# Optimization experiments

Hardware: AMD Instinct MI355X
Metric: run time of the kernel (lower is better)

The kernel has to match this reference:

```python
import jax, jax.numpy as jnp
import numpy as np
from jax import lax

# Fixed high-pass biquad coefficients from SpecTransform.__init__ (a0=b0=1)
A_HP = (-1.99599, 0.996)
B_HP = (-2.0, 1.0)


def _biquad(x, b0, b1, b2, a1, a2):
    """Direct-form-I second-order IIR along last axis of x: (B, T).
    y[t] = b0*x[t] + b1*x[t-1] + b2*x[t-2] - a1*y[t-1] - a2*y[t-2]
    Matches torchaudio.functional.biquad (which calls lfilter with
    default clamp=True, clipping the final output to [-1, 1]).
    """
    z = jnp.zeros((x.shape[0],), x.dtype)

    def step(carry, xt):
        x1, x2, y1, y2 = carry
        y = b0 * xt + b1 * x1 + b2 * x2 - a1 * y1 - a2 * y2
        return (xt, x1, y, y1), y

    _, y = lax.scan(step, (z, z, z, z), x.T)  # scan over time, carry over batch
    return jnp.clip(y.T, -1.0, 1.0)


def _chain(sig, coefs):
    # coefs = [a1, a2, b1, b2] from _rand_resp (hoisted out for determinism)
    a1, a2, b1, b2 = coefs[0], coefs[1], coefs[2], coefs[3]
    sig = _biquad(sig, 1.0, B_HP[0], B_HP[1], A_HP[0], A_HP[1])
    sig = _biquad(sig, 1.0, b1, b2, a1, a2)
    return sig


def setup_inputs() -> dict:
    key = jax.random.key(0)
    k1, k2, k3, k4 = jax.random.split(key, 4)
    B, T = 64, 160000  # 64 clips of 10 s @ 16 kHz
    x = jax.random.normal(k1, (B, T), jnp.float32) * 0.1
    n = jax.random.normal(k2, (B, T), jnp.float32) * 0.1
    # 0.75 * (U[0,1) - 0.5), same distribution as _rand_resp
    coef_x = (jax.random.uniform(k3, (4,), jnp.float32) - 0.5) * 0.75
    coef_n = (jax.random.uniform(k4, (4,), jnp.float32) - 0.5) * 0.75
    return {"x": x, "n": n, "coef_x": coef_x, "coef_n": coef_n}


def reference(x, n, coef_x, coef_n):
    return (_chain(x, coef_x), _chain(n, coef_n))
```

## Files before the change

### kernel.cpp

```cpp
#include <hip/hip_runtime.h>
#include <math.h>

#define T_LEN   160000
#define NROW    128
#define CH      32
#define NCH     5000
#define OWNT    20
#define NCH16   10000
#define OWN16   60
#define B16     240
#define TILES16 42
#define NBLK16  (NROW * TILES16)
#define ROW4    40000

#define C1_HP ( 1.99599)
#define C2_HP (-0.996)
#define C1F   ( 1.99599f)
#define C2F   (-0.996f)

#define S1_FLOAT2S (NROW * NCH)
#define M2_BYTE_OFF (S1_FLOAT2S * 8)

#define GLOBAL_AS __attribute__((address_space(1)))
#define SHARED_AS __attribute__((address_space(3)))

__device__ __forceinline__ int sz16(int F) { return F ^ ((F >> 3) & 7); }
__device__ __forceinline__ float clip1f(float v) { return fminf(fmaxf(v, -1.0f), 1.0f); }

__global__ __launch_bounds__(256) void pass_a1(const float* __restrict__ x,
                                               const float* __restrict__ nn,
                                               float2* __restrict__ e1,
                                               const float* __restrict__ cx,
                                               const float* __restrict__ cn,
                                               float4* __restrict__ m2) {
  int g = blockIdx.x * blockDim.x + threadIdx.x;
  if (g < 2) {
    const float* c = g ? cn : cx;
    const float A1c = c[0], A2c = c[1];
    float pm2 = 0.f, pm1 = 0.f, p0 = 1.f;
#pragma unroll
    for (int k = 0; k < 16; ++k) {
      float pn = -A1c * p0 - A2c * pm1;
      pm2 = pm1; pm1 = p0; p0 = pn;
    }
    float m00 = p0, m01 = -A2c * pm1, m10 = pm1, m11 = -A2c * pm2;
    float q00 = m00*m00 + m01*m10, q01 = m00*m01 + m01*m11;
    float q10 = m10*m00 + m11*m10, q11 = m10*m01 + m11*m11;
    float r00 = q00*m00 + q01*m10, r01 = q00*m01 + q01*m11;
    float r10 = q10*m00 + q11*m10, r11 = q10*m01 + q11*m11;
    m2[g*3 + 0] = make_float4(m00, m01, m10, m11);
    m2[g*3 + 1] = make_float4(q00, q01, q10, q11);
    m2[g*3 + 2] = make_float4(r00, r01, r10, r11);
  }
  if (g >= NROW * NCH) return;
  int row = g / NCH, c = g % NCH;
  const float* src = (row < 64) ? (x + (size_t)row * T_LEN)
                                : (nn + (size_t)(row - 64) * T_LEN);
  const float* xp = src + c * CH;
  float x1 = 0.f, x2 = 0.f;
  if (c) { x1 = xp[-1]; x2 = xp[-2]; }
  double y1 = 0.0, y2 = 0.0;
#pragma unroll
  for (int j = 0; j < CH; j += 4) {
    float4 xv = *reinterpret_cast<const float4*>(xp + j);
#define A1STEP(XF) { float xt = (XF); \
    float fir = (xt - 2.f * x1 + x2); \
    double y = fma(C1_HP, y1, fma(C2_HP, y2, (double)fir)); \
    x2 = x1; x1 = xt; y2 = y1; y1 = y; }
    A1STEP(xv.x) A1STEP(xv.y) A1STEP(xv.z) A1STEP(xv.w)
#undef A1STEP
  }
  e1[g] = make_float2((float)y1, (float)y2);
}

__global__ __launch_bounds__(256) void scan_row(const float2* __restrict__ e,
                                                float2* __restrict__ s) {
  __shared__ double wm[4][6];
  const int t = threadIdx.x, row = blockIdx.x;
  const int lane = t & 63, wv = t >> 6;
  double pm2 = 0.0, pm1 = 0.0, p0 = 1.0;
#pragma unroll
  for (int k = 1; k <= CH; ++k) {
    double pn = C1_HP * p0 + C2_HP * pm1;
    pm2 = pm1; pm1 = p0; p0 = pn;
  }
  const double m00 = p0,  m01 = C2_HP * pm1;
  const double m10 = pm1, m11 = C2_HP * pm2;
  const float2* ep = e + (size_t)row * NCH;
  const int base = t * OWNT;
  double f1 = 0.0, f2 = 0.0;
  for (int j = 0; j < OWNT; ++j) {
    int c = base + j;
    float2 ev = (c < NCH) ? ep[c] : make_float2(0.f, 0.f);
    double n1 = m00 * f1 + m01 * f2 + (double)ev.x;
    double n2 = m10 * f1 + m11 * f2 + (double)ev.y;
    f1 = n1; f2 = n2;
  }
  double b00 = m00, b01 = m01, b10 = m10, b11 = m11;
  double r00 = 1.0, r01 = 0.0, r10 = 0.0, r11 = 1.0;
  int ee = OWNT;
  while (ee) {
    if (ee & 1) {
      double t00 = b00 * r00 + b01 * r10, t01 = b00 * r01 + b01 * r11;
      double t10 = b10 * r00 + b11 * r10, t11 = b10 * r01 + b11 * r11;
      r00 = t00; r01 = t01; r10 = t10; r11 = t11;
    }
    double q00 = b00 * b00 + b01 * b10, q01 = b00 * b01 + b01 * b11;
    double q10 = b10 * b00 + b11 * b10, q11 = b10 * b01 + b11 * b11;
    b00 = q00; b01 = q01; b10 = q10; b11 = q11;
    ee >>= 1;
  }
  double P00 = r00, P01 = r01, P10 = r10, P11 = r11, V1 = f1, V2 = f2;
#pragma unroll
  for (int off = 1; off < 64; off <<= 1) {
    double u00 = __shfl_up(P00, off), u01 = __shfl_up(P01, off);
    double u10 = __shfl_up(P10, off), u11 = __shfl_up(P11, off);
    double uv1 = __shfl_up(V1, off),  uv2 = __shfl_up(V2, off);
    if (lane >= off) {
      double nv1 = P00 * uv1 + P01 * uv2 + V1;
      double nv2 = P10 * uv1 + P11 * uv2 + V2;
      double n00 = P00 * u00 + P01 * u10, n01 = P00 * u01 + P01 * u11;
      double n10 = P10 * u00 + P11 * u10, n11 = P10 * u01 + P11 * u11;
      P00 = n00; P01 = n01; P10 = n10; P11 = n11; V1 = nv1; V2 = nv2;
    }
  }
  if (lane == 63) {
    wm[wv][0] = P00; wm[wv][1] = P01; wm[wv][2] = P10; wm[wv][3] = P11;
    wm[wv][4] = V1;  wm[wv][5] = V2;
  }
  __syncthreads();
  double S1 = 0.0, S2 = 0.0;
  for (int w = 0; w < wv; ++w) {
    double n1 = wm[w][0] * S1 + wm[w][1] * S2 + wm[w][4];
    double n2 = wm[w][2] * S1 + wm[w][3] * S2 + wm[w][5];
    S1 = n1; S2 = n2;
  }
  double q00 = __shfl_up(P00, 1), q01 = __shfl_up(P01, 1);
  double q10 = __shfl_up(P10, 1), q11 = __shfl_up(P11, 1);
  double qv1 = __shfl_up(V1, 1),  qv2 = __shfl_up(V2, 1);
  double st1, st2;
  if (lane == 0) { st1 = S1; st2 = S2; }
  else { st1 = q00 * S1 + q01 * S2 + qv1; st2 = q10 * S1 + q11 * S2 + qv2; }
  float2* sp = s + (size_t)row * NCH;
  double s1v = st1, s2v = st2;
  for (int j = 0; j < OWNT; ++j) {
    int c = base + j;
    if (c < NCH) {
      sp[c] = make_float2((float)s1v, (float)s2v);
      float2 ev = ep[c];
      double n1 = m00 * s1v + m01 * s2v + (double)ev.x;
      double n2 = m10 * s1v + m11 * s2v + (double)ev.y;
      s1v = n1; s2v = n2;
    }
  }
}

__global__ __launch_bounds__(256, 8) void emit_kernel(const float* __restrict__ x,
                                                      const float* __restrict__ nn,
                                                      const float2* __restrict__ s1,
                                                      const float* __restrict__ cx,
                                                      const float* __restrict__ cn,
                                                      const float4* __restrict__ m2,
                                                      float* __restrict__ out) {
  __shared__ float4 ws4[1024];
  const int tid = threadIdx.x, lane = tid & 63, wv = tid >> 6;
  const int b = blockIdx.x;
  const int row = b / TILES16, tile = b % TILES16;
  const int W0 = tile * B16 + wv * OWN16;
  const int c = W0 - 4 + lane;
  const float* src = (row < 64) ? x + (size_t)row * T_LEN
                                : nn + (size_t)(row - 64) * T_LEN;
  const float4* src4 = reinterpret_cast<const float4*>(src);
  const float2* srow = s1 + (size_t)row * NCH;
  const float* cf = (row < 64) ? cx : cn;
  const float A1c = cf[0], A2c = cf[1], B1c = cf[2], B2c = cf[3];
  const int fi = (row < 64) ? 0 : 1;
  const float4 M1q = m2[fi*3], M2q = m2[fi*3+1], M3q = m2[fi*3+2];
  const bool cOK = (c >= 0) && (c < NCH16);

  const int WOFF = wv * 256;
  const long base4 = (long)(W0 - 4) * 4;
  const bool interior = (base4 >= 0) && (base4 + 256 <= ROW4);

  if (interior) {
    const int lane_sz = lane ^ ((lane >> 3) & 7);
#pragma unroll
    for (int q = 0; q < 4; ++q) {
      const float4* gp = src4 + base4 + q * 64 + lane_sz;
      __builtin_amdgcn_global_load_lds(
          (const GLOBAL_AS void*)gp,
          (SHARED_AS void*)(ws4 + WOFF + q * 64),
          16, 0, 0);
    }
    asm volatile("s_waitcnt vmcnt(0)" ::: "memory");
  } else {
#pragma unroll
    for (int q = 0; q < 4; ++q) {
      int f = q * 64 + lane;
      long g4 = base4 + f;
      float4 v = make_float4(0.f, 0.f, 0.f, 0.f);
      if (g4 >= 0 && g4 < ROW4) v = src4[g4];
      ws4[WOFF + sz16(f)] = v;
    }
  }

  float4 a[4];
#pragma unroll
  for (int q = 0; q < 4; ++q) a[q] = ws4[WOFF + sz16(lane * 4 + q)];

  float tx  = __shfl_up(a[3].w, 1), ty  = __shfl_up(a[3].z, 1);
  float t2x = __shfl_up(a[3].w, 2), t2y = __shfl_up(a[3].z, 2);

  float x1 = 0.f, x2 = 0.f, y1 = 0.f, y2 = 0.f, v1 = 0.f, v2 = 0.f;
  if (cOK && c > 0) {
    float2 sv = srow[c >> 1];
    y1 = sv.x; y2 = sv.y;
    if ((lane & 1) == 0) {
      if (lane == 0) {
        float2 tp = *reinterpret_cast<const float2*>(src + (long)c * 16 - 2);
        x2 = tp.x; x1 = tp.y;
      } else { x1 = tx; x2 = ty; }
    } else {
      float ax1 = 0.f, ax2 = 0.f;
      if (lane == 1) {
        if (c >= 2) {
          float2 tp = *reinterpret_cast<const float2*>(src + (long)(c - 1) * 16 - 2);
          ax2 = tp.x; ax1 = tp.y;
        }
      } else { ax1 = t2x; ax2 = t2y; }
      float4 p0 = ws4[WOFF + sz16((lane - 1) * 4 + 0)];
      float4 p1 = ws4[WOFF + sz16((lane - 1) * 4 + 1)];
      float4 p2 = ws4[WOFF + sz16((lane - 1) * 4 + 2)];
      float4 p3 = ws4[WOFF + sz16((lane - 1) * 4 + 3)];
#define ADV(XT) { float xt_ = (XT); \
      float fir = (xt_ - 2.f * ax1 + ax2); \
      float yy = fmaf(C1F, y1, fmaf(C2F, y2, fir)); \
      ax2 = ax1; ax1 = xt_; y2 = y1; y1 = yy; }
      ADV(p0.x) ADV(p0.y) ADV(p0.z) ADV(p0.w)
      ADV(p1.x) ADV(p1.y) ADV(p1.z) ADV(p1.w)
      ADV(p2.x) ADV(p2.y) ADV(p2.z) ADV(p2.w)
      ADV(p3.x) ADV(p3.y) ADV(p3.z) ADV(p3.w)
#undef ADV
      x1 = ax1; x2 = ax2;
    }
    v1 = clip1f(y1); v2 = clip1f(y2);
  }

  {
    float xp1 = x1, xp2 = x2;
#pragma unroll
    for (int q = 0; q < 4; ++q) {
      float4 t = a[q];
      float4 f;
      f.x = t.x - 2.f * xp1 + xp2;
      f.y = t.y - 2.f * t.x + xp1;
      f.z = t.z - 2.f * t.y + t.x;
      f.w = t.w - 2.f * t.z + t.y;
      xp2 = t.z; xp1 = t.w;
      a[q] = f;
    }
  }

  float z1 = 0.f, z2 = 0.f;
  if (cOK) {
#define AB(REF) { \
    float yy = fmaf(C1F, y1, fmaf(C2F, y2, (REF))); \
    float vv = clip1f(yy); \
    float zz = fmaf(-A1c, z1, fmaf(-A2c, z2, fmaf(B2c, v2, fmaf(B1c, v1, vv)))); \
    y2 = y1; y1 = yy; v2 = v1; v1 = vv; z2 = z1; z1 = zz; REF = zz; }
#pragma unroll
    for (int q = 0; q < 4; ++q) { AB(a[q].x) AB(a[q].y) AB(a[q].z) AB(a[q].w) }
#undef AB
  }

  float u1x = __shfl_up(z1, 1), u1y = __shfl_up(z2, 1);
  float u2x = __shfl_up(z1, 2), u2y = __shfl_up(z2, 2);
  float u3x = __shfl_up(z1, 3), u3y = __shfl_up(z2, 3);
  float u4x = __shfl_up(z1, 4), u4y = __shfl_up(z2, 4);

  if (lane >= 4 && cOK) {
    float s2x = 0.f, s2y = 0.f;
    if (c >= 1) { s2x = u1x; s2y = u1y; }
    if (c >= 2) { s2x = fmaf(M1q.x, u2x, fmaf(M1q.y, u2y, s2x));
                  s2y = fmaf(M1q.z, u2x, fmaf(M1q.w, u2y, s2y)); }
    if (c >= 3) { s2x = fmaf(M2q.x, u3x, fmaf(M2q.y, u3y, s2x));
                  s2y = fmaf(M2q.z, u3x, fmaf(M2q.w, u3y, s2y)); }
    if (c >= 4) { s2x = fmaf(M3q.x, u4x, fmaf(M3q.y, u4y, s2x));
                  s2y = fmaf(M3q.z, u4x, fmaf(M3q.w, u4y, s2y)); }
    float h1 = s2x, h2 = s2y;
#define CS(ZB, OT) { float hh = fmaf(-A1c, h1, -A2c * h2); \
    OT = clip1f((ZB) + hh); h2 = h1; h1 = hh; }
#pragma unroll
    for (int q = 0; q < 4; ++q) {
      float4 o;
      CS(a[q].x, o.x) CS(a[q].y, o.y) CS(a[q].z, o.z) CS(a[q].w, o.w)
      ws4[WOFF + sz16(lane * 4 + q)] = o;
    }
#undef CS
  }

  float* orow = out + (size_t)row * T_LEN;
#pragma unroll
  for (int q = 0; q < 4; ++q) {
    int f = q * 64 + lane;
    long g4 = base4 + f;
    if (f >= 16 && g4 < ROW4)
      reinterpret_cast<float4*>(orow)[g4] = ws4[WOFF + sz16(f)];
  }
}

extern "C" void kernel_launch(void* const* d_in, const int* in_sizes, int n_in,
                              void* d_out, int out_size, void* d_ws, size_t ws_size,
                              hipStream_t stream) {
  const float* x  = (const float*)d_in[0];
  const float* nn = (const float*)d_in[1];
  const float* cx = (const float*)d_in[2];
  const float* cn = (const float*)d_in[3];
  float* out = (float*)d_out;

  float2* e1 = (float2*)d_out;
  float2* s1 = (float2*)d_ws;
  float4* m2 = (float4*)((char*)d_ws + M2_BYTE_OFF);

  const int total = NROW * NCH;
  const int blk = 256;
  const int nb = (total + blk - 1) / blk;

  pass_a1<<<nb, blk, 0, stream>>>(x, nn, e1, cx, cn, m2);
  scan_row<<<NROW, blk, 0, stream>>>(e1, s1);
  emit_kernel<<<NBLK16, blk, 0, stream>>>(x, nn, s1, cx, cn, m2, out);
}
```

Measured before the change: 62.91 us.

## Process two sub-tiles per wave with overlapped async LDS loads in emit kernel

```diff
diff --git a/kernel.cpp b/kernel.cpp
--- a/kernel.cpp
+++ b/kernel.cpp
@@ -8,8 +8,9 @@
 #define OWNT    20
 #define NCH16   10000
 #define OWN16   60
-#define B16     240
-#define TILES16 42
+#define WAVE_OWN 120
+#define B16     480
+#define TILES16 21
 #define NBLK16  (NROW * TILES16)
 #define ROW4    40000
 
@@ -155,19 +156,31 @@
   }
 }
 
-__global__ __launch_bounds__(256, 8) void emit_kernel(const float* __restrict__ x,
+#define ABSTEP(REF) { \
+    float yy = fmaf(C1F, y1, fmaf(C2F, y2, (REF))); \
+    float vv = clip1f(yy); \
+    float zz = fmaf(-A1c, z1, fmaf(-A2c, z2, fmaf(B2c, v2, fmaf(B1c, v1, vv)))); \
+    y2 = y1; y1 = yy; v2 = v1; v1 = vv; z2 = z1; z1 = zz; REF = zz; }
+#define CSSTEP(ZB, OT) { float hh = fmaf(-A1c, h1, -A2c * h2); \
+    OT = clip1f((ZB) + hh); h2 = h1; h1 = hh; }
+#define ADVSTEP(XT) { float xt_ = (XT); \
+    float fir = (xt_ - 2.f * ax1 + ax2); \
+    float yy = fmaf(C1F, y1, fmaf(C2F, y2, fir)); \
+    ax2 = ax1; ax1 = xt_; y2 = y1; y1 = yy; }
+
+__global__ __launch_bounds__(256, 5) void emit_kernel(const float* __restrict__ x,
                                                       const float* __restrict__ nn,
                                                       const float2* __restrict__ s1,
                                                       const float* __restrict__ cx,
                                                       const float* __restrict__ cn,
                                                       const float4* __restrict__ m2,
                                                       float* __restrict__ out) {
-  __shared__ float4 ws4[1024];
+  __shared__ float4 ws4[2048];
   const int tid = threadIdx.x, lane = tid & 63, wv = tid >> 6;
   const int b = blockIdx.x;
   const int row = b / TILES16, tile = b % TILES16;
-  const int W0 = tile * B16 + wv * OWN16;
-  const int c = W0 - 4 + lane;
+  const int W0a = tile * B16 + wv * WAVE_OWN;
+  const int W0b = W0a + OWN16;
   const float* src = (row < 64) ? x + (size_t)row * T_LEN
                                 : nn + (size_t)(row - 64) * T_LEN;
   const float4* src4 = reinterpret_cast<const float4*>(src);
@@ -176,138 +189,152 @@
   const float A1c = cf[0], A2c = cf[1], B1c = cf[2], B2c = cf[3];
   const int fi = (row < 64) ? 0 : 1;
   const float4 M1q = m2[fi*3], M2q = m2[fi*3+1], M3q = m2[fi*3+2];
-  const bool cOK = (c >= 0) && (c < NCH16);
-
-  const int WOFF = wv * 256;
-  const long base4 = (long)(W0 - 4) * 4;
-  const bool interior = (base4 >= 0) && (base4 + 256 <= ROW4);
-
-  if (interior) {
-    const int lane_sz = lane ^ ((lane >> 3) & 7);
-#pragma unroll
-    for (int q = 0; q < 4; ++q) {
-      const float4* gp = src4 + base4 + q * 64 + lane_sz;
-      __builtin_amdgcn_global_load_lds(
-          (const GLOBAL_AS void*)gp,
-          (SHARED_AS void*)(ws4 + WOFF + q * 64),
-          16, 0, 0);
-    }
-    asm volatile("s_waitcnt vmcnt(0)" ::: "memory");
-  } else {
+
+  const int ca = W0a - 4 + lane, cb = W0b - 4 + lane;
+  const bool okA = (ca >= 0) && (ca < NCH16);
+  const bool okB = (cb >= 0) && (cb < NCH16);
+  const long b4a = (long)(W0a - 4) * 4, b4b = (long)(W0b - 4) * 4;
+  const int WOFFa = wv * 512, WOFFb = wv * 512 + 256;
+  const bool intA = (b4a >= 0) && (b4a + 256 <= ROW4);
+  const bool intB = (b4b >= 0) && (b4b + 256 <= ROW4);
+
+  float2 svA = make_float2(0.f, 0.f), svB = make_float2(0.f, 0.f);
+  if (okA && ca > 0) svA = srow[ca >> 1];
+  if (okB && cb > 0) svB = srow[cb >> 1];
+  float2 tpA = make_float2(0.f, 0.f), tqA = make_float2(0.f, 0.f);
+  float2 tpB = make_float2(0.f, 0.f), tqB = make_float2(0.f, 0.f);
+  if (lane == 0) {
+    if (okA && ca > 0) tpA = *reinterpret_cast<const float2*>(src + (long)ca * 16 - 2);
+    if (okB && cb > 0) tpB = *reinterpret_cast<const float2*>(src + (long)cb * 16 - 2);
+  }
+  if (lane == 1) {
+    if (okA && ca >= 2) tqA = *reinterpret_cast<const float2*>(src + (long)(ca - 1) * 16 - 2);
+    if (okB && cb >= 2) tqB = *reinterpret_cast<const float2*>(src + (long)(cb - 1) * 16 - 2);
+  }
+
+  auto process = [&](int c, bool cOK, long base4, int WOFF,
+                     float2 sv, float2 tp, float2 tq) {
+    float4 a[4];
+#pragma unroll
+    for (int q = 0; q < 4; ++q) a[q] = ws4[WOFF + sz16(lane * 4 + q)];
+    float tx  = __shfl_up(a[3].w, 1), ty  = __shfl_up(a[3].z, 1);
+    float t2x = __shfl_up(a[3].w, 2), t2y = __shfl_up(a[3].z, 2);
+    float x1 = 0.f, x2 = 0.f, y1 = 0.f, y2 = 0.f, v1 = 0.f, v2 = 0.f;
+    if (cOK && c > 0) {
+      y1 = sv.x; y2 = sv.y;
+      if ((lane & 1) == 0) {
+        if (lane == 0) { x2 = tp.x; x1 = tp.y; }
+        else { x1 = tx; x2 = ty; }
+      } else {
+        float ax1 = 0.f, ax2 = 0.f;
+        if (lane == 1) { if (c >= 2) { ax2 = tq.x; ax1 = tq.y; } }
+        else { ax1 = t2x; ax2 = t2y; }
+        float4 p0 = ws4[WOFF + sz16((lane - 1) * 4 + 0)];
+        float4 p1 = ws4[WOFF + sz16((lane - 1) * 4 + 1)];
+        float4 p2 = ws4[WOFF + sz16((lane - 1) * 4 + 2)];
+        float4 p3 = ws4[WOFF + sz16((lane - 1) * 4 + 3)];
+        ADVSTEP(p0.x) ADVSTEP(p0.y) ADVSTEP(p0.z) ADVSTEP(p0.w)
+        ADVSTEP(p1.x) ADVSTEP(p1.y) ADVSTEP(p1.z) ADVSTEP(p1.w)
+        ADVSTEP(p2.x) ADVSTEP(p2.y) ADVSTEP(p2.z) ADVSTEP(p2.w)
+        ADVSTEP(p3.x) ADVSTEP(p3.y) ADVSTEP(p3.z) ADVSTEP(p3.w)
+        x1 = ax1; x2 = ax2;
+      }
+      v1 = clip1f(y1); v2 = clip1f(y2);
+    }
+    {
+      float xp1 = x1, xp2 = x2;
+#pragma unroll
+      for (int q = 0; q < 4; ++q) {
+        float4 t = a[q];
+        float4 f;
+        f.x = t.x - 2.f * xp1 + xp2;
+        f.y = t.y - 2.f * t.x + xp1;
+        f.z = t.z - 2.f * t.y + t.x;
+        f.w = t.w - 2.f * t.z + t.y;
+        xp2 = t.z; xp1 = t.w;
+        a[q] = f;
+      }
+    }
+    float z1 = 0.f, z2 = 0.f;
+    if (cOK) {
+#pragma unroll
+      for (int q = 0; q < 4; ++q) {
+        ABSTEP(a[q].x) ABSTEP(a[q].y) ABSTEP(a[q].z) ABSTEP(a[q].w)
+      }
+    }
+    float u1x = __shfl_up(z1, 1), u1y = __shfl_up(z2, 1);
+    float u2x = __shfl_up(z1, 2), u2y = __shfl_up(z2, 2);
+    float u3x = __shfl_up(z1, 3), u3y = __shfl_up(z2, 3);
+    float u4x = __shfl_up(z1, 4), u4y = __shfl_up(z2, 4);
+    if (lane >= 4 && cOK) {
+      float s2x = 0.f, s2y = 0.f;
+      if (c >= 1) { s2x = u1x; s2y = u1y; }
+      if (c >= 2) { s2x = fmaf(M1q.x, u2x, fmaf(M1q.y, u2y, s2x));
+                    s2y = fmaf(M1q.z, u2x, fmaf(M1q.w, u2y, s2y)); }
+      if (c >= 3) { s2x = fmaf(M2q.x, u3x, fmaf(M2q.y, u3y, s2x));
+                    s2y = fmaf(M2q.z, u3x, fmaf(M2q.w, u3y, s2y)); }
+      if (c >= 4) { s2x = fmaf(M3q.x, u4x, fmaf(M3q.y, u4y, s2x));
+                    s2y = fmaf(M3q.z, u4x, fmaf(M3q.w, u4y, s2y)); }
+      float h1 = s2x, h2 = s2y;
+#pragma unroll
+      for (int q = 0; q < 4; ++q) {
+        float4 o;
+        CSSTEP(a[q].x, o.x) CSSTEP(a[q].y, o.y)
+        CSSTEP(a[q].z, o.z) CSSTEP(a[q].w, o.w)
+        ws4[WOFF + sz16(lane * 4 + q)] = o;
+      }
+    }
+    float* orow = out + (size_t)row * T_LEN;
 #pragma unroll
     for (int q = 0; q < 4; ++q) {
       int f = q * 64 + lane;
       long g4 = base4 + f;
+      if (f >= 16 && g4 < ROW4)
+        reinterpret_cast<float4*>(orow)[g4] = ws4[WOFF + sz16(f)];
+    }
+  };
+
+  if (intA && intB) {
+    const int lane_sz = lane ^ ((lane >> 3) & 7);
+#pragma unroll
+    for (int q = 0; q < 4; ++q)
+      __builtin_amdgcn_global_load_lds(
+          (const GLOBAL_AS void*)(src4 + b4a + q * 64 + lane_sz),
+          (SHARED_AS void*)(ws4 + WOFFa + q * 64), 16, 0, 0);
+#pragma unroll
+    for (int q = 0; q < 4; ++q)
+      __builtin_amdgcn_global_load_lds(
+          (const GLOBAL_AS void*)(src4 + b4b + q * 64 + lane_sz),
+          (SHARED_AS void*)(ws4 + WOFFb + q * 64), 16, 0, 0);
+    asm volatile("s_waitcnt vmcnt(4)" ::: "memory");
+    process(ca, okA, b4a, WOFFa, svA, tpA, tqA);
+    asm volatile("s_waitcnt vmcnt(4)" ::: "memory");
+    process(cb, okB, b4b, WOFFb, svB, tpB, tqB);
+  } else {
+#pragma unroll
+    for (int q = 0; q < 4; ++q) {
+      int f = q * 64 + lane;
+      long g4 = b4a + f;
       float4 v = make_float4(0.f, 0.f, 0.f, 0.f);
       if (g4 >= 0 && g4 < ROW4) v = src4[g4];
-      ws4[WOFF + sz16(f)] = v;
-    }
-  }
-
-  float4 a[4];
-#pragma unroll
-  for (int q = 0; q < 4; ++q) a[q] = ws4[WOFF + sz16(lane * 4 + q)];
-
-  float tx  = __shfl_up(a[3].w, 1), ty  = __shfl_up(a[3].z, 1);
-  float t2x = __shfl_up(a[3].w, 2), t2y = __shfl_up(a[3].z, 2);
-
-  float x1 = 0.f, x2 = 0.f, y1 = 0.f, y2 = 0.f, v1 = 0.f, v2 = 0.f;
-  if (cOK && c > 0) {
-    float2 sv = srow[c >> 1];
-    y1 = sv.x; y2 = sv.y;
-    if ((lane & 1) == 0) {
-      if (lane == 0) {
-        float2 tp = *reinterpret_cast<const float2*>(src + (long)c * 16 - 2);
-        x2 = tp.x; x1 = tp.y;
-      } else { x1 = tx; x2 = ty; }
-    } else {
-      float ax1 = 0.f, ax2 = 0.f;
-      if (lane == 1) {
-        if (c >= 2) {
-          float2 tp = *reinterpret_cast<const float2*>(src + (long)(c - 1) * 16 - 2);
-          ax2 = tp.x; ax1 = tp.y;
-        }
-      } else { ax1 = t2x; ax2 = t2y; }
-      float4 p0 = ws4[WOFF + sz16((lane - 1) * 4 + 0)];
-      float4 p1 = ws4[WOFF + sz16((lane - 1) * 4 + 1)];
-      float4 p2 = ws4[WOFF + sz16((lane - 1) * 4 + 2)];
-      float4 p3 = ws4[WOFF + sz16((lane - 1) * 4 + 3)];
-#define ADV(XT) { float xt_ = (XT); \
-      float fir = (xt_ - 2.f * ax1 + ax2); \
-      float yy = fmaf(C1F, y1, fmaf(C2F, y2, fir)); \
-      ax2 = ax1; ax1 = xt_; y2 = y1; y1 = yy; }
-      ADV(p0.x) ADV(p0.y) ADV(p0.z) ADV(p0.w)
-      ADV(p1.x) ADV(p1.y) ADV(p1.z) ADV(p1.w)
-      ADV(p2.x) ADV(p2.y) ADV(p2.z) ADV(p2.w)
-      ADV(p3.x) ADV(p3.y) ADV(p3.z) ADV(p3.w)
-#undef ADV
-      x1 = ax1; x2 = ax2;
-    }
-    v1 = clip1f(y1); v2 = clip1f(y2);
-  }
-
-  {
-    float xp1 = x1, xp2 = x2;
+      ws4[WOFFa + sz16(f)] = v;
+    }
+    process(ca, okA, b4a, WOFFa, svA, tpA, tqA);
 #pragma unroll
     for (int q = 0; q < 4; ++q) {
-      float4 t = a[q];
-      float4 f;
-      f.x = t.x - 2.f * xp1 + xp2;
-      f.y = t.y - 2.f * t.x + xp1;
-      f.z = t.z - 2.f * t.y + t.x;
-      f.w = t.w - 2.f * t.z + t.y;
-      xp2 = t.z; xp1 = t.w;
-      a[q] = f;
-    }
-  }
-
-  float z1 = 0.f, z2 = 0.f;
-  if (cOK) {
-#define AB(REF) { \
-    float yy = fmaf(C1F, y1, fmaf(C2F, y2, (REF))); \
-    float vv = clip1f(yy); \
-    float zz = fmaf(-A1c, z1, fmaf(-A2c, z2, fmaf(B2c, v2, fmaf(B1c, v1, vv)))); \
-    y2 = y1; y1 = yy; v2 = v1; v1 = vv; z2 = z1; z1 = zz; REF = zz; }
-#pragma unroll
-    for (int q = 0; q < 4; ++q) { AB(a[q].x) AB(a[q].y) AB(a[q].z) AB(a[q].w) }
-#undef AB
-  }
-
-  float u1x = __shfl_up(z1, 1), u1y = __shfl_up(z2, 1);
-  float u2x = __shfl_up(z1, 2), u2y = __shfl_up(z2, 2);
-  float u3x = __shfl_up(z1, 3), u3y = __shfl_up(z2, 3);
-  float u4x = __shfl_up(z1, 4), u4y = __shfl_up(z2, 4);
-
-  if (lane >= 4 && cOK) {
-    float s2x = 0.f, s2y = 0.f;
-    if (c >= 1) { s2x = u1x; s2y = u1y; }
-    if (c >= 2) { s2x = fmaf(M1q.x, u2x, fmaf(M1q.y, u2y, s2x));
-                  s2y = fmaf(M1q.z, u2x, fmaf(M1q.w, u2y, s2y)); }
-    if (c >= 3) { s2x = fmaf(M2q.x, u3x, fmaf(M2q.y, u3y, s2x));
-                  s2y = fmaf(M2q.z, u3x, fmaf(M2q.w, u3y, s2y)); }
-    if (c >= 4) { s2x = fmaf(M3q.x, u4x, fmaf(M3q.y, u4y, s2x));
-                  s2y = fmaf(M3q.z, u4x, fmaf(M3q.w, u4y, s2y)); }
-    float h1 = s2x, h2 = s2y;
-#define CS(ZB, OT) { float hh = fmaf(-A1c, h1, -A2c * h2); \
-    OT = clip1f((ZB) + hh); h2 = h1; h1 = hh; }
-#pragma unroll
-    for (int q = 0; q < 4; ++q) {
-      float4 o;
-      CS(a[q].x, o.x) CS(a[q].y, o.y) CS(a[q].z, o.z) CS(a[q].w, o.w)
-      ws4[WOFF + sz16(lane * 4 + q)] = o;
-    }
-#undef CS
-  }
-
-  float* orow = out + (size_t)row * T_LEN;
-#pragma unroll
-  for (int q = 0; q < 4; ++q) {
-    int f = q * 64 + lane;
-    long g4 = base4 + f;
-    if (f >= 16 && g4 < ROW4)
-      reinterpret_cast<float4*>(orow)[g4] = ws4[WOFF + sz16(f)];
+      int f = q * 64 + lane;
+      long g4 = b4b + f;
+      float4 v = make_float4(0.f, 0.f, 0.f, 0.f);
+      if (g4 >= 0 && g4 < ROW4) v = src4[g4];
+      ws4[WOFFb + sz16(f)] = v;
+    }
+    process(cb, okB, b4b, WOFFb, svB, tpB, tqB);
   }
 }
+
+#undef ABSTEP
+#undef CSSTEP
+#undef ADVSTEP
 
 extern "C" void kernel_launch(void* const* d_in, const int* in_sizes, int n_in,
                               void* d_out, int out_size, void* d_ws, size_t ws_size,
```

Result: faster. 61.08 us (-2.9%).
